# Kernel tuning notes

Hardware: AMD Instinct MI355X
Metric: run time of the kernel (lower is better)

The kernel has to match this reference:

```python
import jax, jax.numpy as jnp
import numpy as np

L, N, DIN, DOUT = 24, 8192, 256, 128  # levels, nodes/level, dim_in(=2*dim_out), dim_out


def setup_inputs() -> dict:
    key = jax.random.key(0)
    ks = jax.random.split(key, 6)
    s = 1.0 / np.sqrt(DIN)
    tensor = jax.random.normal(ks[0], (L, N, DIN), jnp.float32)
    # child indices into previous level's nodes; -1 == missing child -> learned init state
    indices = jax.random.randint(ks[1], (L, N, 2), -1, N).astype(jnp.int32)
    W_w = jax.random.uniform(ks[2], (4 * DOUT, DIN), jnp.float32, -s, s)
    W_b = jax.random.uniform(ks[3], (4 * DOUT,), jnp.float32, -s, s)
    U_f1 = jax.random.uniform(ks[4], (DOUT, 2 * DOUT), jnp.float32, -s, s)
    U_f2 = jax.random.uniform(jax.random.fold_in(ks[4], 1), (DOUT, 2 * DOUT), jnp.float32, -s, s)
    U_iuo = jax.random.uniform(ks[5], (3 * DOUT, 2 * DOUT), jnp.float32, -s, s)
    h_init = jnp.zeros((1, DOUT), jnp.float32)
    c_init = jnp.zeros((1, DOUT), jnp.float32)
    return dict(tensor=tensor, indices=indices, h_init=h_init, c_init=c_init,
                W_w=W_w, W_b=W_b, U_f1=U_f1, U_f2=U_f2, U_iuo=U_iuo)


def reference(tensor, indices, h_init, c_init, W_w, W_b, U_f1, U_f2, U_iuo):
    D = DOUT

    def step(carry, inp):
        h_prev, c_prev = carry                      # [N, D] each (previous level)
        x, idx = inp                                # x:[N,DIN], idx:[N,2]
        h_ext = jnp.concatenate([h_init, h_prev], axis=0)  # row 0 = init (index -1)
        c_ext = jnp.concatenate([c_init, c_prev], axis=0)
        rows = idx + 1                              # -1 -> 0 (init state)
        h = h_ext[rows]                             # [N, 2, D] gathered child hiddens
        c = c_ext[rows]                             # [N, 2, D]
        W_x = x @ W_w.T + W_b                       # [N, 4D]
        f_x, i_x, u_x, o_x = jnp.split(W_x, 4, axis=1)
        hc = h.reshape(h.shape[0], 2 * D)           # [N, 2D]
        f1 = jax.nn.sigmoid(f_x + hc @ U_f1.T)
        f2 = jax.nn.sigmoid(f_x + hc @ U_f2.T)
        iuo = hc @ U_iuo.T                          # [N, 3D]
        i = jax.nn.sigmoid(iuo[:, :D] + i_x)
        u = jnp.tanh(iuo[:, D:2 * D] + u_x)
        o = jax.nn.sigmoid(iuo[:, 2 * D:] + o_x)
        new_c = i * u + f1 * c[:, 0] + f2 * c[:, 1]
        new_h = o * jnp.tanh(new_c)
        return (new_h, new_c), (new_h, new_c)

    n = tensor.shape[1]
    h0 = jnp.broadcast_to(h_init, (n, D))
    c0 = jnp.broadcast_to(c_init, (n, D))
    _, (res_h, res_c) = jax.lax.scan(step, (h0, c0), (tensor, indices))
    return res_h, res_c                              # each [L, N, D]
```

## Files before the change

### kernel.cpp

```cpp
#include <hip/hip_runtime.h>
#include <stdint.h>

#define LVL 24
#define NN  8192
#define DIN 256
#define DD  128
#define BM  32
#define NBLK 512
#define CSW 66

typedef __attribute__((ext_vector_type(8))) short bf16x8;
typedef __attribute__((ext_vector_type(4))) float f32x4;

__device__ __forceinline__ float b2f(unsigned short u) {
    union { unsigned int i; float f; } v; v.i = ((unsigned int)u) << 16; return v.f;
}
__device__ __forceinline__ unsigned short f2b(float f) {
    union { float f; unsigned int i; } v; v.f = f;
    unsigned int x = v.i;
    return (unsigned short)((x + 0x7fffu + ((x >> 16) & 1u)) >> 16);
}
__device__ __forceinline__ float sig_(float x) { return 1.0f / (1.0f + __expf(-x)); }

__device__ __forceinline__ float ldf(const void* p, size_t i, int isf) {
    return isf ? ((const float*)p)[i] : b2f(((const unsigned short*)p)[i]);
}

__global__ void detect_kernel(const unsigned short* __restrict__ t, int* __restrict__ flag) {
    __shared__ int cnt;
    if (threadIdx.x == 0) cnt = 0;
    __syncthreads();
    int bad = 0;
    #pragma unroll
    for (int r = 0; r < 4; ++r) {
        unsigned short u = t[(threadIdx.x * 4 + r) * 2];
        int e = (u >> 7) & 255;
        bad += (e >= 136 || (e >= 1 && e <= 90)) ? 1 : 0;
    }
    atomicAdd(&cnt, bad);
    __syncthreads();
    if (threadIdx.x == 0) *flag = (cnt > 16) ? 1 : 0;
}

__global__ __launch_bounds__(256)
void convert_kernel(const void* Ww, const void* Wb, const void* Uf1, const void* Uf2,
                    const void* Uiuo, const void* hini, const void* cini,
                    unsigned short* __restrict__ wpack, float* __restrict__ bias,
                    unsigned short* __restrict__ hinit_b, float* __restrict__ cinit_f,
                    unsigned int* __restrict__ bar,
                    const int* __restrict__ flag) {
    const int isf = *flag;
    const int bid = blockIdx.x;
    const int t = threadIdx.x;
    if (bid < 1152) {
        const int row = bid, col = t;
        float v;
        if (row < 512)       v = ldf(Ww,   (size_t)row * DIN + col, isf);
        else if (row < 640)  v = ldf(Uf1,  (size_t)(row - 512) * DIN + col, isf);
        else if (row < 768)  v = ldf(Uf2,  (size_t)(row - 640) * DIN + col, isf);
        else                 v = ldf(Uiuo, (size_t)(row - 768) * DIN + col, isf);
        const int g  = row >> 7;
        const int wr = row & 127;
        const int dt = wr >> 4;
        const int mm = wr & 15;
        const int kk = col >> 5;
        const int q  = (col >> 3) & 3;
        const int j  = col & 7;
        const size_t pos = (size_t)((g * 8 + dt) * 8 + kk) * 512 + (q * 16 + mm) * 8 + j;
        wpack[pos] = f2b(v);
    } else if (bid == 1152) {
        bias[t] = ldf(Wb, t, isf);
    } else if (bid == 1153) {
        bias[256 + t] = ldf(Wb, 256 + t, isf);
    } else if (bid == 1154) {
        if (t < 128) hinit_b[t] = f2b(ldf(hini, t, isf));
        else if (t < 256) cinit_f[t - 128] = ldf(cini, t - 128, isf);
    } else {
        for (int i = t; i < 320; i += 256) bar[i] = 0u;
    }
}

__device__ __forceinline__ void stage_x_tile(unsigned short* __restrict__ xsbuf,
                                             const void* __restrict__ xbase,
                                             int level, int bm, int tid, int isf) {
    const int u0 = tid >> 4;
    const int r0 = tid & 15;
    #pragma unroll
    for (int du = 0; du < 2; ++du) {
        const int u = u0 + du * 16;
        const int kk = u >> 2, qq = u & 3;
        #pragma unroll
        for (int dr = 0; dr < 2; ++dr) {
            const int r = r0 + dr * 16;
            const size_t re = (size_t)level * NN * DIN + (size_t)(bm * BM + r) * DIN + u * 8;
            union { unsigned short us[8]; uint4 v; } t;
            if (isf) {
                const float4* xr = (const float4*)((const float*)xbase + re);
                float4 v0 = xr[0], v1 = xr[1];
                t.us[0] = f2b(v0.x); t.us[1] = f2b(v0.y); t.us[2] = f2b(v0.z); t.us[3] = f2b(v0.w);
                t.us[4] = f2b(v1.x); t.us[5] = f2b(v1.y); t.us[6] = f2b(v1.z); t.us[7] = f2b(v1.w);
            } else {
                t.v = *(const uint4*)((const unsigned short*)xbase + re);
            }
            *(uint4*)&xsbuf[kk * 1024 + qq * 256 + r * 8] = t.v;
        }
    }
}

__device__ __forceinline__ void lean_barrier(unsigned int* __restrict__ bar, int lvl, int bid) {
    __syncthreads();
    if (threadIdx.x == 0) {
        __builtin_amdgcn_fence(__ATOMIC_RELEASE, "agent");
        const int slot = bid & 7;
        unsigned int prev = __hip_atomic_fetch_add(&bar[slot * 32], 1u,
                                                   __ATOMIC_RELAXED, __HIP_MEMORY_SCOPE_AGENT);
        if (prev + 1u == (unsigned int)(64 * (lvl + 1))) {
            unsigned int mp = __hip_atomic_fetch_add(&bar[8 * 32], 1u,
                                                     __ATOMIC_RELAXED, __HIP_MEMORY_SCOPE_AGENT);
            if (mp + 1u == (unsigned int)(8 * (lvl + 1))) {
                __hip_atomic_store(&bar[9 * 32], (unsigned int)(lvl + 1),
                                   __ATOMIC_RELEASE, __HIP_MEMORY_SCOPE_AGENT);
            }
        }
        while (__hip_atomic_load(&bar[9 * 32], __ATOMIC_RELAXED,
                                 __HIP_MEMORY_SCOPE_AGENT) < (unsigned int)(lvl + 1))
            __builtin_amdgcn_s_sleep(8);
        __builtin_amdgcn_fence(__ATOMIC_ACQUIRE, "agent");
    }
    __syncthreads();
}

__global__ __launch_bounds__(256, 2)
void fused_kernel(const void* __restrict__ xbase,
                  const int* __restrict__ idxall,
                  unsigned short* __restrict__ hb0,
                  unsigned short* __restrict__ hb1,
                  float* __restrict__ out,
                  const unsigned short* __restrict__ wpack,
                  const float* __restrict__ bias,
                  const unsigned short* __restrict__ hinit_b,
                  const float* __restrict__ cinit_f,
                  const int* __restrict__ flag,
                  unsigned int* __restrict__ bar) {
    __shared__ unsigned short xs[2][8192];
    __shared__ unsigned short hs[8192];
    __shared__ float cs[64 * CSW];

    const int tid = threadIdx.x;
    const int isf = *flag;
    const int bid = blockIdx.x;
    const int bm  = bid & 255;
    const int yh  = bid >> 8;

    const int lane = tid & 63;
    const int wave = tid >> 6;
    const int m    = lane & 15;
    const int q    = lane >> 4;
    const int dt   = yh * 4 + wave;
    const int d    = yh * 64 + wave * 16 + m;
    const int dloc = wave * 16 + m;
    const unsigned short* wb = wpack + (size_t)dt * 4096 + (size_t)lane * 8;
    const float bfv = bias[d], biv = bias[128 + d], buv = bias[256 + d], bov = bias[384 + d];
    const float ci_init = cinit_f[d];

    const int gr  = tid & 31;
    const int gsp = tid >> 5;
    const int gs    = gsp >> 2;
    const int gpart = gsp & 3;

    stage_x_tile(xs[0], xbase, 0, bm, tid, isf);

    for (int l = 0; l < LVL; ++l) {
        const int first = (l == 0) ? 1 : 0;
        const int* __restrict__ idx = idxall + (size_t)l * NN * 2;
        const unsigned short* __restrict__ hprev = (l & 1) ? hb1 : hb0;
        unsigned short* __restrict__ hnew        = (l & 1) ? hb0 : hb1;
        const float* __restrict__ cprev = out + (size_t)(LVL + l - 1) * NN * DD;
        float* __restrict__ outh = out + (size_t)l * NN * DD;
        float* __restrict__ outc = out + (size_t)(LVL + l) * NN * DD;

        {
            const int ai = idx[(bm * BM + gr) * 2 + gs];
            const int use_init = (first || ai < 0);

            const unsigned short* hsrc = use_init ? (hinit_b + gpart * 32)
                                                  : (hprev + (size_t)ai * DD + gpart * 32);
            const int kk = gs * 4 + gpart;
            #pragma unroll
            for (int qq = 0; qq < 4; ++qq)
                *(uint4*)&hs[kk * 1024 + qq * 256 + gr * 8] = ((const uint4*)hsrc)[qq];

            const float* csrc = use_init ? (cinit_f + yh * 64 + gpart * 16)
                                         : (cprev + (size_t)ai * DD + yh * 64 + gpart * 16);
            float* cdst = &cs[(gs * 32 + gr) * CSW + gpart * 16];
            #pragma unroll
            for (int qq = 0; qq < 4; ++qq)
                ((float4*)cdst)[qq] = ((const float4*)csrc)[qq];
        }
        __syncthreads();

        const unsigned short* __restrict__ xcur = xs[l & 1];
        f32x4 acc[9][2];
        #pragma unroll
        for (int g = 0; g < 9; ++g) { acc[g][0] = (f32x4)0.0f; acc[g][1] = (f32x4)0.0f; }

        #pragma unroll
        for (int kk = 0; kk < 8; ++kk) {
            const int xo = kk * 1024 + q * 256 + m * 8;
            bf16x8 a0 = *(const bf16x8*)&xcur[xo];
            bf16x8 a1 = *(const bf16x8*)&xcur[xo + 128];
            bf16x8 h0 = *(const bf16x8*)&hs[xo];
            bf16x8 h1 = *(const bf16x8*)&hs[xo + 128];
            #pragma unroll
            for (int g = 0; g < 4; ++g) {
                bf16x8 b = *(const bf16x8*)(wb + (size_t)g * 32768 + kk * 512);
                acc[g][0] = __builtin_amdgcn_mfma_f32_16x16x32_bf16(a0, b, acc[g][0], 0, 0, 0);
                acc[g][1] = __builtin_amdgcn_mfma_f32_16x16x32_bf16(a1, b, acc[g][1], 0, 0, 0);
            }
            #pragma unroll
            for (int g = 4; g < 9; ++g) {
                bf16x8 b = *(const bf16x8*)(wb + (size_t)g * 32768 + kk * 512);
                acc[g][0] = __builtin_amdgcn_mfma_f32_16x16x32_bf16(h0, b, acc[g][0], 0, 0, 0);
                acc[g][1] = __builtin_amdgcn_mfma_f32_16x16x32_bf16(h1, b, acc[g][1], 0, 0, 0);
            }
        }

        if (l + 1 < LVL)
            stage_x_tile(xs[(l + 1) & 1], xbase, l + 1, bm, tid, isf);

        #pragma unroll
        for (int mt = 0; mt < 2; ++mt) {
            #pragma unroll
            for (int j = 0; j < 4; ++j) {
                const int rr = mt * 16 + q * 4 + j;
                const int nd = bm * BM + rr;
                const float ca = cs[rr * CSW + dloc];
                const float cb = cs[(32 + rr) * CSW + dloc];
                const float fx = acc[0][mt][j] + bfv;
                const float ix = acc[1][mt][j] + biv;
                const float ux = acc[2][mt][j] + buv;
                const float ox = acc[3][mt][j] + bov;
                const float f1 = sig_(fx + acc[4][mt][j]);
                const float f2 = sig_(fx + acc[5][mt][j]);
                const float ig = sig_(ix + acc[6][mt][j]);
                const float ug = tanhf(ux + acc[7][mt][j]);
                const float og = sig_(ox + acc[8][mt][j]);
                const float nc = ig * ug + f1 * ca + f2 * cb;
                const float nh = og * tanhf(nc);
                const size_t o = (size_t)nd * DD + d;
                hnew[o] = f2b(nh);
                outh[o] = nh;
                outc[o] = nc;
            }
        }

        if (l + 1 < LVL) lean_barrier(bar, l, bid);
    }
}

__global__ __launch_bounds__(256, 3)
void level_kernel(const void* __restrict__ xbase, int level,
                  const int* __restrict__ idx,
                  const unsigned short* __restrict__ hprev,
                  const float* __restrict__ cprev,
                  unsigned short* __restrict__ hnew,
                  float* __restrict__ outh,
                  float* __restrict__ outc,
                  const unsigned short* __restrict__ wpack,
                  const float* __restrict__ bias,
                  const unsigned short* __restrict__ hinit_b,
                  const float* __restrict__ cinit_f,
                  const int* __restrict__ flag,
                  int first) {
    __shared__ unsigned short xs[8192];
    __shared__ unsigned short hs[8192];
    __shared__ float cs[64 * CSW];

    const int tid = threadIdx.x;
    const int isf = *flag;
    const int bm  = blockIdx.x;
    const int yh  = blockIdx.y;

    stage_x_tile(xs, xbase, level, bm, tid, isf);
    {
        const int r  = tid & 31;
        const int sp = tid >> 5;
        const int s    = sp >> 2;
        const int part = sp & 3;
        const int ai = idx[(bm * BM + r) * 2 + s];
        const int use_init = (first || ai < 0);

        const unsigned short* hsrc = use_init ? (hinit_b + part * 32)
                                              : (hprev + (size_t)ai * DD + part * 32);
        const int kk = s * 4 + part;
        #pragma unroll
        for (int qq = 0; qq < 4; ++qq)
            *(uint4*)&hs[kk * 1024 + qq * 256 + r * 8] = ((const uint4*)hsrc)[qq];

        const float* csrc = use_init ? (cinit_f + yh * 64 + part * 16)
                                     : (cprev + (size_t)ai * DD + yh * 64 + part * 16);
        float* cdst = &cs[(s * 32 + r) * CSW + part * 16];
        #pragma unroll
        for (int qq = 0; qq < 4; ++qq)
            ((float4*)cdst)[qq] = ((const float4*)csrc)[qq];
    }
    __syncthreads();

    const int lane = tid & 63;
    const int wave = tid >> 6;
    const int m    = lane & 15;
    const int q    = lane >> 4;
    const int dt   = yh * 4 + wave;
    const int d    = yh * 64 + wave * 16 + m;
    const unsigned short* wb = wpack + (size_t)dt * 4096 + (size_t)lane * 8;

    f32x4 acc[9][2];
    #pragma unroll
    for (int g = 0; g < 9; ++g) { acc[g][0] = (f32x4)0.0f; acc[g][1] = (f32x4)0.0f; }

    #pragma unroll
    for (int kk = 0; kk < 8; ++kk) {
        const int xo = kk * 1024 + q * 256 + m * 8;
        bf16x8 a0 = *(const bf16x8*)&xs[xo];
        bf16x8 a1 = *(const bf16x8*)&xs[xo + 128];
        bf16x8 h0 = *(const bf16x8*)&hs[xo];
        bf16x8 h1 = *(const bf16x8*)&hs[xo + 128];
        #pragma unroll
        for (int g = 0; g < 4; ++g) {
            bf16x8 b = *(const bf16x8*)(wb + (size_t)g * 32768 + kk * 512);
            acc[g][0] = __builtin_amdgcn_mfma_f32_16x16x32_bf16(a0, b, acc[g][0], 0, 0, 0);
            acc[g][1] = __builtin_amdgcn_mfma_f32_16x16x32_bf16(a1, b, acc[g][1], 0, 0, 0);
        }
        #pragma unroll
        for (int g = 4; g < 9; ++g) {
            bf16x8 b = *(const bf16x8*)(wb + (size_t)g * 32768 + kk * 512);
            acc[g][0] = __builtin_amdgcn_mfma_f32_16x16x32_bf16(h0, b, acc[g][0], 0, 0, 0);
            acc[g][1] = __builtin_amdgcn_mfma_f32_16x16x32_bf16(h1, b, acc[g][1], 0, 0, 0);
        }
    }

    const float bfv = bias[d], biv = bias[128 + d], buv = bias[256 + d], bov = bias[384 + d];
    const int dloc = wave * 16 + m;
    #pragma unroll
    for (int mt = 0; mt < 2; ++mt) {
        #pragma unroll
        for (int j = 0; j < 4; ++j) {
            const int rr = mt * 16 + q * 4 + j;
            const int nd = bm * BM + rr;
            const float ca = cs[rr * CSW + dloc];
            const float cb = cs[(32 + rr) * CSW + dloc];
            const float fx = acc[0][mt][j] + bfv;
            const float ix = acc[1][mt][j] + biv;
            const float ux = acc[2][mt][j] + buv;
            const float ox = acc[3][mt][j] + bov;
            const float f1 = sig_(fx + acc[4][mt][j]);
            const float f2 = sig_(fx + acc[5][mt][j]);
            const float ig = sig_(ix + acc[6][mt][j]);
            const float ug = tanhf(ux + acc[7][mt][j]);
            const float og = sig_(ox + acc[8][mt][j]);
            const float nc = ig * ug + f1 * ca + f2 * cb;
            const float nh = og * tanhf(nc);
            const size_t o = (size_t)nd * DD + d;
            hnew[o] = f2b(nh);
            outh[o] = nh;
            outc[o] = nc;
        }
    }
}

extern "C" void kernel_launch(void* const* d_in, const int* in_sizes, int n_in,
                              void* d_out, int out_size, void* d_ws, size_t ws_size,
                              hipStream_t stream) {
    const void* tensor  = d_in[0];
    const int*  indices = (const int*)d_in[1];
    const void* h_init  = d_in[2];
    const void* c_init  = d_in[3];
    const void* Ww      = d_in[4];
    const void* Wb      = d_in[5];
    const void* Uf1     = d_in[6];
    const void* Uf2     = d_in[7];
    const void* Uiuo    = d_in[8];
    float* out = (float*)d_out;

    char* wsb = (char*)d_ws;
    int* flag                = (int*)wsb;
    unsigned short* wpack    = (unsigned short*)(wsb + 256);
    float* bias              = (float*)(wsb + 590336);
    unsigned short* hinit_b  = (unsigned short*)(wsb + 592640);
    float* cinit_f           = (float*)(wsb + 593152);
    unsigned int* bar        = (unsigned int*)(wsb + 594176);
    unsigned short* hb0      = (unsigned short*)(wsb + (1u << 20));
    unsigned short* hb1      = (unsigned short*)(wsb + (1u << 20) + 2097152);

    detect_kernel<<<1, 64, 0, stream>>>((const unsigned short*)tensor, flag);
    convert_kernel<<<1156, 256, 0, stream>>>(Ww, Wb, Uf1, Uf2, Uiuo, h_init, c_init,
                                             wpack, bias, hinit_b, cinit_f, bar, flag);

    static int nb = -1;
    if (nb < 0) {
        if (hipOccupancyMaxActiveBlocksPerMultiprocessor(&nb, fused_kernel, 256, 0)
            != hipSuccess) nb = 0;
    }

    if (nb >= 2) {
        void* kargs[] = { (void*)&tensor, (void*)&indices, (void*)&hb0, (void*)&hb1,
                          (void*)&out, (void*)&wpack, (void*)&bias, (void*)&hinit_b,
                          (void*)&cinit_f, (void*)&flag, (void*)&bar };
        hipLaunchCooperativeKernel((const void*)fused_kernel, dim3(NBLK), dim3(256),
                                   kargs, 0, stream);
    } else {
        unsigned short* hp = hb0;
        unsigned short* hn = hb1;
        for (int l = 0; l < LVL; ++l) {
            const float* cprev = (l == 0) ? (const float*)out
                                          : (const float*)(out + (size_t)(LVL + l - 1) * NN * DD);
            level_kernel<<<dim3(NN / BM, 2), 256, 0, stream>>>(
                tensor, l,
                indices + (size_t)l * NN * 2,
                hp, cprev, hn,
                out + (size_t)l * NN * DD,
                out + (size_t)(LVL + l) * NN * DD,
                wpack, bias, hinit_b, cinit_f, flag, (l == 0) ? 1 : 0);
            unsigned short* th = hp; hp = hn; hn = th;
        }
    }
}
```

Measured before the change: 751.7 us.

## Replace grid barrier with per-tile readiness flags and 512-thread full-width blocks

The persistent kernel now runs one 512-thread block per 32-node tile covering all 128 output dims, instead of two 256-thread blocks per tile. The global per-level barrier is replaced with per-tile ready flags, so each thread waits only for the producer tile of its child index. The x-part MFMAs are issued before the child-state gather to overlap latency, and child h/c are read from the fp32 output rather than a separate bf16 buffer. tanhf is replaced by an exp-based tanh; the risks are the relaxed-atomic flag publish ordering and reduced occupancy from larger blocks.

```diff
diff --git a/kernel.cpp b/kernel.cpp
--- a/kernel.cpp
+++ b/kernel.cpp
@@ -6,8 +6,8 @@
 #define DIN 256
 #define DD  128
 #define BM  32
-#define NBLK 512
-#define CSW 66
+#define NT  (NN / BM)
+#define CSW 132
 
 typedef __attribute__((ext_vector_type(8))) short bf16x8;
 typedef __attribute__((ext_vector_type(4))) float f32x4;
@@ -21,9 +21,15 @@
     return (unsigned short)((x + 0x7fffu + ((x >> 16) & 1u)) >> 16);
 }
 __device__ __forceinline__ float sig_(float x) { return 1.0f / (1.0f + __expf(-x)); }
-
+__device__ __forceinline__ float tanh_(float x) {
+    float e = __expf(2.0f * x);
+    return (e - 1.0f) / (e + 1.0f);
+}
 __device__ __forceinline__ float ldf(const void* p, size_t i, int isf) {
     return isf ? ((const float*)p)[i] : b2f(((const unsigned short*)p)[i]);
+}
+__device__ __forceinline__ void st_agent(float* p, float v) {
+    __hip_atomic_store(p, v, __ATOMIC_RELAXED, __HIP_MEMORY_SCOPE_AGENT);
 }
 
 __global__ void detect_kernel(const unsigned short* __restrict__ t, int* __restrict__ flag) {
@@ -47,7 +53,7 @@
                     const void* Uiuo, const void* hini, const void* cini,
                     unsigned short* __restrict__ wpack, float* __restrict__ bias,
                     unsigned short* __restrict__ hinit_b, float* __restrict__ cinit_f,
-                    unsigned int* __restrict__ bar,
+                    unsigned int* __restrict__ rdy,
                     const int* __restrict__ flag) {
     const int isf = *flag;
     const int bid = blockIdx.x;
@@ -76,147 +82,136 @@
         if (t < 128) hinit_b[t] = f2b(ldf(hini, t, isf));
         else if (t < 256) cinit_f[t - 128] = ldf(cini, t - 128, isf);
     } else {
-        for (int i = t; i < 320; i += 256) bar[i] = 0u;
-    }
-}
-
-__device__ __forceinline__ void stage_x_tile(unsigned short* __restrict__ xsbuf,
-                                             const void* __restrict__ xbase,
-                                             int level, int bm, int tid, int isf) {
-    const int u0 = tid >> 4;
-    const int r0 = tid & 15;
+        for (int i = t; i < LVL * NT; i += 256) rdy[i] = 0u;
+    }
+}
+
+__device__ __forceinline__ void stage_x512(unsigned short* __restrict__ xsbuf,
+                                           const void* __restrict__ xbase,
+                                           int level, int tile, int tid, int isf) {
+    const int r  = tid & 31;
+    const int u0 = tid >> 5;
     #pragma unroll
     for (int du = 0; du < 2; ++du) {
         const int u = u0 + du * 16;
         const int kk = u >> 2, qq = u & 3;
-        #pragma unroll
-        for (int dr = 0; dr < 2; ++dr) {
-            const int r = r0 + dr * 16;
-            const size_t re = (size_t)level * NN * DIN + (size_t)(bm * BM + r) * DIN + u * 8;
-            union { unsigned short us[8]; uint4 v; } t;
-            if (isf) {
-                const float4* xr = (const float4*)((const float*)xbase + re);
-                float4 v0 = xr[0], v1 = xr[1];
-                t.us[0] = f2b(v0.x); t.us[1] = f2b(v0.y); t.us[2] = f2b(v0.z); t.us[3] = f2b(v0.w);
-                t.us[4] = f2b(v1.x); t.us[5] = f2b(v1.y); t.us[6] = f2b(v1.z); t.us[7] = f2b(v1.w);
-            } else {
-                t.v = *(const uint4*)((const unsigned short*)xbase + re);
-            }
-            *(uint4*)&xsbuf[kk * 1024 + qq * 256 + r * 8] = t.v;
-        }
-    }
-}
-
-__device__ __forceinline__ void lean_barrier(unsigned int* __restrict__ bar, int lvl, int bid) {
-    __syncthreads();
-    if (threadIdx.x == 0) {
-        __builtin_amdgcn_fence(__ATOMIC_RELEASE, "agent");
-        const int slot = bid & 7;
-        unsigned int prev = __hip_atomic_fetch_add(&bar[slot * 32], 1u,
-                                                   __ATOMIC_RELAXED, __HIP_MEMORY_SCOPE_AGENT);
-        if (prev + 1u == (unsigned int)(64 * (lvl + 1))) {
-            unsigned int mp = __hip_atomic_fetch_add(&bar[8 * 32], 1u,
-                                                     __ATOMIC_RELAXED, __HIP_MEMORY_SCOPE_AGENT);
-            if (mp + 1u == (unsigned int)(8 * (lvl + 1))) {
-                __hip_atomic_store(&bar[9 * 32], (unsigned int)(lvl + 1),
-                                   __ATOMIC_RELEASE, __HIP_MEMORY_SCOPE_AGENT);
-            }
-        }
-        while (__hip_atomic_load(&bar[9 * 32], __ATOMIC_RELAXED,
-                                 __HIP_MEMORY_SCOPE_AGENT) < (unsigned int)(lvl + 1))
-            __builtin_amdgcn_s_sleep(8);
-        __builtin_amdgcn_fence(__ATOMIC_ACQUIRE, "agent");
-    }
-    __syncthreads();
-}
-
-__global__ __launch_bounds__(256, 2)
+        const size_t re = (size_t)level * NN * DIN + (size_t)(tile * BM + r) * DIN + u * 8;
+        union { unsigned short us[8]; uint4 v; } t;
+        if (isf) {
+            const float4* xr = (const float4*)((const float*)xbase + re);
+            float4 v0 = xr[0], v1 = xr[1];
+            t.us[0] = f2b(v0.x); t.us[1] = f2b(v0.y); t.us[2] = f2b(v0.z); t.us[3] = f2b(v0.w);
+            t.us[4] = f2b(v1.x); t.us[5] = f2b(v1.y); t.us[6] = f2b(v1.z); t.us[7] = f2b(v1.w);
+        } else {
+            t.v = *(const uint4*)((const unsigned short*)xbase + re);
+        }
+        *(uint4*)&xsbuf[kk * 1024 + qq * 256 + r * 8] = t.v;
+    }
+}
+
+__global__ __launch_bounds__(512, 2)
 void fused_kernel(const void* __restrict__ xbase,
                   const int* __restrict__ idxall,
-                  unsigned short* __restrict__ hb0,
-                  unsigned short* __restrict__ hb1,
                   float* __restrict__ out,
                   const unsigned short* __restrict__ wpack,
                   const float* __restrict__ bias,
                   const unsigned short* __restrict__ hinit_b,
                   const float* __restrict__ cinit_f,
                   const int* __restrict__ flag,
-                  unsigned int* __restrict__ bar) {
+                  unsigned int* __restrict__ rdy) {
     __shared__ unsigned short xs[2][8192];
     __shared__ unsigned short hs[8192];
     __shared__ float cs[64 * CSW];
 
-    const int tid = threadIdx.x;
-    const int isf = *flag;
-    const int bid = blockIdx.x;
-    const int bm  = bid & 255;
-    const int yh  = bid >> 8;
+    const int tid  = threadIdx.x;
+    const int isf  = *flag;
+    const int tile = blockIdx.x;
+
+    const int gr = tid & 31;
+    const int gs = (tid >> 5) & 1;
+    const int p2 = tid >> 6;
 
     const int lane = tid & 63;
-    const int wave = tid >> 6;
+    const int dt   = tid >> 6;
     const int m    = lane & 15;
     const int q    = lane >> 4;
-    const int dt   = yh * 4 + wave;
-    const int d    = yh * 64 + wave * 16 + m;
-    const int dloc = wave * 16 + m;
+    const int d    = dt * 16 + m;
     const unsigned short* wb = wpack + (size_t)dt * 4096 + (size_t)lane * 8;
     const float bfv = bias[d], biv = bias[128 + d], buv = bias[256 + d], bov = bias[384 + d];
-    const float ci_init = cinit_f[d];
-
-    const int gr  = tid & 31;
-    const int gsp = tid >> 5;
-    const int gs    = gsp >> 2;
-    const int gpart = gsp & 3;
-
-    stage_x_tile(xs[0], xbase, 0, bm, tid, isf);
+
+    stage_x512(xs[0], xbase, 0, tile, tid, isf);
+    int ai = idxall[(size_t)(tile * BM + gr) * 2 + gs];
 
     for (int l = 0; l < LVL; ++l) {
-        const int first = (l == 0) ? 1 : 0;
-        const int* __restrict__ idx = idxall + (size_t)l * NN * 2;
-        const unsigned short* __restrict__ hprev = (l & 1) ? hb1 : hb0;
-        unsigned short* __restrict__ hnew        = (l & 1) ? hb0 : hb1;
-        const float* __restrict__ cprev = out + (size_t)(LVL + l - 1) * NN * DD;
-        float* __restrict__ outh = out + (size_t)l * NN * DD;
-        float* __restrict__ outc = out + (size_t)(LVL + l) * NN * DD;
-
-        {
-            const int ai = idx[(bm * BM + gr) * 2 + gs];
-            const int use_init = (first || ai < 0);
-
-            const unsigned short* hsrc = use_init ? (hinit_b + gpart * 32)
-                                                  : (hprev + (size_t)ai * DD + gpart * 32);
-            const int kk = gs * 4 + gpart;
-            #pragma unroll
-            for (int qq = 0; qq < 4; ++qq)
-                *(uint4*)&hs[kk * 1024 + qq * 256 + gr * 8] = ((const uint4*)hsrc)[qq];
-
-            const float* csrc = use_init ? (cinit_f + yh * 64 + gpart * 16)
-                                         : (cprev + (size_t)ai * DD + yh * 64 + gpart * 16);
-            float* cdst = &cs[(gs * 32 + gr) * CSW + gpart * 16];
-            #pragma unroll
-            for (int qq = 0; qq < 4; ++qq)
-                ((float4*)cdst)[qq] = ((const float4*)csrc)[qq];
-        }
-        __syncthreads();
+        const int use_init = (l == 0) || (ai < 0);
+
+        if (l > 0 && ai >= 0) {
+            const unsigned int* fp = &rdy[(size_t)(l - 1) * NT + (ai >> 5)];
+            while (__hip_atomic_load(fp, __ATOMIC_RELAXED, __HIP_MEMORY_SCOPE_AGENT) == 0u)
+                __builtin_amdgcn_s_sleep(1);
+        }
+        asm volatile("" ::: "memory");
+
+        float4 hv0, hv1, hv2, hv3, cv0, cv1, cv2, cv3;
+        if (use_init) {
+            const unsigned short* hi = hinit_b + p2 * 16;
+            hv0 = make_float4(b2f(hi[0]), b2f(hi[1]), b2f(hi[2]), b2f(hi[3]));
+            hv1 = make_float4(b2f(hi[4]), b2f(hi[5]), b2f(hi[6]), b2f(hi[7]));
+            hv2 = make_float4(b2f(hi[8]), b2f(hi[9]), b2f(hi[10]), b2f(hi[11]));
+            hv3 = make_float4(b2f(hi[12]), b2f(hi[13]), b2f(hi[14]), b2f(hi[15]));
+            const float4* ci = (const float4*)(cinit_f + p2 * 16);
+            cv0 = ci[0]; cv1 = ci[1]; cv2 = ci[2]; cv3 = ci[3];
+        } else {
+            const float4* hrow = (const float4*)(out + (size_t)(l - 1) * NN * DD
+                                                 + (size_t)ai * DD + p2 * 16);
+            hv0 = hrow[0]; hv1 = hrow[1]; hv2 = hrow[2]; hv3 = hrow[3];
+            const float4* crow = (const float4*)(out + (size_t)(LVL + l - 1) * NN * DD
+                                                 + (size_t)ai * DD + p2 * 16);
+            cv0 = crow[0]; cv1 = crow[1]; cv2 = crow[2]; cv3 = crow[3];
+        }
 
         const unsigned short* __restrict__ xcur = xs[l & 1];
         f32x4 acc[9][2];
         #pragma unroll
         for (int g = 0; g < 9; ++g) { acc[g][0] = (f32x4)0.0f; acc[g][1] = (f32x4)0.0f; }
-
         #pragma unroll
         for (int kk = 0; kk < 8; ++kk) {
             const int xo = kk * 1024 + q * 256 + m * 8;
             bf16x8 a0 = *(const bf16x8*)&xcur[xo];
             bf16x8 a1 = *(const bf16x8*)&xcur[xo + 128];
-            bf16x8 h0 = *(const bf16x8*)&hs[xo];
-            bf16x8 h1 = *(const bf16x8*)&hs[xo + 128];
             #pragma unroll
             for (int g = 0; g < 4; ++g) {
                 bf16x8 b = *(const bf16x8*)(wb + (size_t)g * 32768 + kk * 512);
                 acc[g][0] = __builtin_amdgcn_mfma_f32_16x16x32_bf16(a0, b, acc[g][0], 0, 0, 0);
                 acc[g][1] = __builtin_amdgcn_mfma_f32_16x16x32_bf16(a1, b, acc[g][1], 0, 0, 0);
             }
+        }
+
+        {
+            unsigned int w0 = (unsigned int)f2b(hv0.x) | ((unsigned int)f2b(hv0.y) << 16);
+            unsigned int w1 = (unsigned int)f2b(hv0.z) | ((unsigned int)f2b(hv0.w) << 16);
+            unsigned int w2 = (unsigned int)f2b(hv1.x) | ((unsigned int)f2b(hv1.y) << 16);
+            unsigned int w3 = (unsigned int)f2b(hv1.z) | ((unsigned int)f2b(hv1.w) << 16);
+            unsigned int w4 = (unsigned int)f2b(hv2.x) | ((unsigned int)f2b(hv2.y) << 16);
+            unsigned int w5 = (unsigned int)f2b(hv2.z) | ((unsigned int)f2b(hv2.w) << 16);
+            unsigned int w6 = (unsigned int)f2b(hv3.x) | ((unsigned int)f2b(hv3.y) << 16);
+            unsigned int w7 = (unsigned int)f2b(hv3.z) | ((unsigned int)f2b(hv3.w) << 16);
+            const int u0 = gs * 16 + p2 * 2;
+            const int u1 = u0 + 1;
+            *(uint4*)&hs[(u0 >> 2) * 1024 + (u0 & 3) * 256 + gr * 8] =
+                make_uint4(w0, w1, w2, w3);
+            *(uint4*)&hs[(u1 >> 2) * 1024 + (u1 & 3) * 256 + gr * 8] =
+                make_uint4(w4, w5, w6, w7);
+            float4* cd = (float4*)&cs[(gs * 32 + gr) * CSW + p2 * 16];
+            cd[0] = cv0; cd[1] = cv1; cd[2] = cv2; cd[3] = cv3;
+        }
+        __syncthreads();
+
+        #pragma unroll
+        for (int kk = 0; kk < 8; ++kk) {
+            const int xo = kk * 1024 + q * 256 + m * 8;
+            bf16x8 h0 = *(const bf16x8*)&hs[xo];
+            bf16x8 h1 = *(const bf16x8*)&hs[xo + 128];
             #pragma unroll
             for (int g = 4; g < 9; ++g) {
                 bf16x8 b = *(const bf16x8*)(wb + (size_t)g * 32768 + kk * 512);
@@ -225,17 +220,21 @@
             }
         }
 
-        if (l + 1 < LVL)
-            stage_x_tile(xs[(l + 1) & 1], xbase, l + 1, bm, tid, isf);
-
+        if (l + 1 < LVL) {
+            stage_x512(xs[(l + 1) & 1], xbase, l + 1, tile, tid, isf);
+            ai = idxall[(size_t)(l + 1) * NN * 2 + (size_t)(tile * BM + gr) * 2 + gs];
+        }
+
+        float* __restrict__ outh = out + (size_t)l * NN * DD;
+        float* __restrict__ outc = out + (size_t)(LVL + l) * NN * DD;
         #pragma unroll
         for (int mt = 0; mt < 2; ++mt) {
             #pragma unroll
             for (int j = 0; j < 4; ++j) {
                 const int rr = mt * 16 + q * 4 + j;
-                const int nd = bm * BM + rr;
-                const float ca = cs[rr * CSW + dloc];
-                const float cb = cs[(32 + rr) * CSW + dloc];
+                const int nd = tile * BM + rr;
+                const float ca = cs[rr * CSW + d];
+                const float cb = cs[(32 + rr) * CSW + d];
                 const float fx = acc[0][mt][j] + bfv;
                 const float ix = acc[1][mt][j] + biv;
                 const float ux = acc[2][mt][j] + buv;
@@ -243,18 +242,20 @@
                 const float f1 = sig_(fx + acc[4][mt][j]);
                 const float f2 = sig_(fx + acc[5][mt][j]);
                 const float ig = sig_(ix + acc[6][mt][j]);
-                const float ug = tanhf(ux + acc[7][mt][j]);
+                const float ug = tanh_(ux + acc[7][mt][j]);
                 const float og = sig_(ox + acc[8][mt][j]);
                 const float nc = ig * ug + f1 * ca + f2 * cb;
-                const float nh = og * tanhf(nc);
+                const float nh = og * tanh_(nc);
                 const size_t o = (size_t)nd * DD + d;
-                hnew[o] = f2b(nh);
-                outh[o] = nh;
-                outc[o] = nc;
+                st_agent(&outh[o], nh);
+                st_agent(&outc[o], nc);
             }
         }
 
-        if (l + 1 < LVL) lean_barrier(bar, l, bid);
+        __syncthreads();
+        if (tid == 0)
+            __hip_atomic_store(&rdy[(size_t)l * NT + tile], 1u,
+                               __ATOMIC_RELAXED, __HIP_MEMORY_SCOPE_AGENT);
     }
 }
 
@@ -272,16 +273,39 @@
                   const float* __restrict__ cinit_f,
                   const int* __restrict__ flag,
                   int first) {
-    __shared__ unsigned short xs[8192];
-    __shared__ unsigned short hs[8192];
-    __shared__ float cs[64 * CSW];
+    __shared__ unsigned short xsl[8192];
+    __shared__ unsigned short hsl[8192];
+    __shared__ float csl[64 * 66];
 
     const int tid = threadIdx.x;
     const int isf = *flag;
     const int bm  = blockIdx.x;
     const int yh  = blockIdx.y;
 
-    stage_x_tile(xs, xbase, level, bm, tid, isf);
+    {
+        const int u0 = tid >> 4;
+        const int r0 = tid & 15;
+        #pragma unroll
+        for (int du = 0; du < 2; ++du) {
+            const int u = u0 + du * 16;
+            const int kk = u >> 2, qq = u & 3;
+            #pragma unroll
+            for (int dr = 0; dr < 2; ++dr) {
+                const int r = r0 + dr * 16;
+                const size_t re = (size_t)level * NN * DIN + (size_t)(bm * BM + r) * DIN + u * 8;
+                union { unsigned short us[8]; uint4 v; } t;
+                if (isf) {
+                    const float4* xr = (const float4*)((const float*)xbase + re);
+                    float4 v0 = xr[0], v1 = xr[1];
+                    t.us[0] = f2b(v0.x); t.us[1] = f2b(v0.y); t.us[2] = f2b(v0.z); t.us[3] = f2b(v0.w);
+                    t.us[4] = f2b(v1.x); t.us[5] = f2b(v1.y); t.us[6] = f2b(v1.z); t.us[7] = f2b(v1.w);
+                } else {
+                    t.v = *(const uint4*)((const unsigned short*)xbase + re);
+                }
+                *(uint4*)&xsl[kk * 1024 + qq * 256 + r * 8] = t.v;
+            }
+        }
+    }
     {
         const int r  = tid & 31;
         const int sp = tid >> 5;
@@ -295,11 +319,11 @@
         const int kk = s * 4 + part;
         #pragma unroll
         for (int qq = 0; qq < 4; ++qq)
-            *(uint4*)&hs[kk * 1024 + qq * 256 + r * 8] = ((const uint4*)hsrc)[qq];
+            *(uint4*)&hsl[kk * 1024 + qq * 256 + r * 8] = ((const uint4*)hsrc)[qq];
 
         const float* csrc = use_init ? (cinit_f + yh * 64 + part * 16)
                                      : (cprev + (size_t)ai * DD + yh * 64 + part * 16);
-        float* cdst = &cs[(s * 32 + r) * CSW + part * 16];
+        float* cdst = &csl[(s * 32 + r) * 66 + part * 16];
         #pragma unroll
         for (int qq = 0; qq < 4; ++qq)
             ((float4*)cdst)[qq] = ((const float4*)csrc)[qq];
@@ -321,10 +345,10 @@
     #pragma unroll
     for (int kk = 0; kk < 8; ++kk) {
         const int xo = kk * 1024 + q * 256 + m * 8;
-        bf16x8 a0 = *(const bf16x8*)&xs[xo];
-        bf16x8 a1 = *(const bf16x8*)&xs[xo + 128];
-        bf16x8 h0 = *(const bf16x8*)&hs[xo];
-        bf16x8 h1 = *(const bf16x8*)&hs[xo + 128];
+        bf16x8 a0 = *(const bf16x8*)&xsl[xo];
+        bf16x8 a1 = *(const bf16x8*)&xsl[xo + 128];
+        bf16x8 h0 = *(const bf16x8*)&hsl[xo];
+        bf16x8 h1 = *(const bf16x8*)&hsl[xo + 128];
         #pragma unroll
         for (int g = 0; g < 4; ++g) {
             bf16x8 b = *(const bf16x8*)(wb + (size_t)g * 32768 + kk * 512);
@@ -347,8 +371,8 @@
         for (int j = 0; j < 4; ++j) {
             const int rr = mt * 16 + q * 4 + j;
             const int nd = bm * BM + rr;
-            const float ca = cs[rr * CSW + dloc];
-            const float cb = cs[(32 + rr) * CSW + dloc];
+            const float ca = csl[rr * 66 + dloc];
+            const float cb = csl[(32 + rr) * 66 + dloc];
             const float fx = acc[0][mt][j] + bfv;
             const float ix = acc[1][mt][j] + biv;
             const float ux = acc[2][mt][j] + buv;
@@ -356,10 +380,10 @@
             const float f1 = sig_(fx + acc[4][mt][j]);
             const float f2 = sig_(fx + acc[5][mt][j]);
             const float ig = sig_(ix + acc[6][mt][j]);
-            const float ug = tanhf(ux + acc[7][mt][j]);
+            const float ug = tanh_(ux + acc[7][mt][j]);
             const float og = sig_(ox + acc[8][mt][j]);
             const float nc = ig * ug + f1 * ca + f2 * cb;
-            const float nh = og * tanhf(nc);
+            const float nh = og * tanh_(nc);
             const size_t o = (size_t)nd * DD + d;
             hnew[o] = f2b(nh);
             outh[o] = nh;
@@ -388,25 +412,25 @@
     float* bias              = (float*)(wsb + 590336);
     unsigned short* hinit_b  = (unsigned short*)(wsb + 592640);
     float* cinit_f           = (float*)(wsb + 593152);
-    unsigned int* bar        = (unsigned int*)(wsb + 594176);
+    unsigned int* rdy        = (unsigned int*)(wsb + 593920);
     unsigned short* hb0      = (unsigned short*)(wsb + (1u << 20));
     unsigned short* hb1      = (unsigned short*)(wsb + (1u << 20) + 2097152);
 
     detect_kernel<<<1, 64, 0, stream>>>((const unsigned short*)tensor, flag);
     convert_kernel<<<1156, 256, 0, stream>>>(Ww, Wb, Uf1, Uf2, Uiuo, h_init, c_init,
-                                             wpack, bias, hinit_b, cinit_f, bar, flag);
+                                             wpack, bias, hinit_b, cinit_f, rdy, flag);
 
     static int nb = -1;
     if (nb < 0) {
-        if (hipOccupancyMaxActiveBlocksPerMultiprocessor(&nb, fused_kernel, 256, 0)
+        if (hipOccupancyMaxActiveBlocksPerMultiprocessor(&nb, fused_kernel, 512, 0)
             != hipSuccess) nb = 0;
     }
 
-    if (nb >= 2) {
-        void* kargs[] = { (void*)&tensor, (void*)&indices, (void*)&hb0, (void*)&hb1,
-                          (void*)&out, (void*)&wpack, (void*)&bias, (void*)&hinit_b,
-                          (void*)&cinit_f, (void*)&flag, (void*)&bar };
-        hipLaunchCooperativeKernel((const void*)fused_kernel, dim3(NBLK), dim3(256),
+    if (nb >= 1) {
+        void* kargs[] = { (void*)&tensor, (void*)&indices, (void*)&out, (void*)&wpack,
+                          (void*)&bias, (void*)&hinit_b, (void*)&cinit_f, (void*)&flag,
+                          (void*)&rdy };
+        hipLaunchCooperativeKernel((const void*)fused_kernel, dim3(NT), dim3(512),
                                    kargs, 0, stream);
     } else {
         unsigned short* hp = hb0;
```

New measurement: 767.4 us. 2.1% more time.
